# Kernel tuning notes

Measured on AMD Instinct MI355X. Metric: run time of the kernel, lower is better.

## Reference

```python
import jax, jax.numpy as jnp
import numpy as np

D_MODEL = 2048
N_HEAD = 16
D_HEAD = D_MODEL // N_HEAD


def setup_inputs() -> dict:
    key = jax.random.key(0)
    k_x, k_qkv, k_proj = jax.random.split(key, 3)
    x = jax.random.normal(k_x, (2, 2048, D_MODEL), dtype=jnp.float32)
    # nn.Linear weights: out = x @ W.T ; store as [out, in] like torch
    scale = 1.0 / np.sqrt(D_MODEL)
    W_qkv = jax.random.uniform(k_qkv, (3 * D_MODEL, D_MODEL), jnp.float32, -scale, scale)
    W_proj = jax.random.uniform(k_proj, (D_MODEL, D_MODEL), jnp.float32, -scale, scale)
    return {"x": x, "W_qkv": W_qkv, "W_proj": W_proj}


def reference(x, W_qkv, W_proj):
    B, T, C = x.shape
    qkv = jnp.einsum('btc,oc->bto', x, W_qkv)  # [B,T,3C]
    q, k, v = jnp.split(qkv, 3, axis=-1)
    def heads(t):
        return t.reshape(B, T, N_HEAD, D_HEAD).transpose(0, 2, 1, 3)  # [B,H,T,Dh]
    q, k, v = heads(q), heads(k), heads(v)
    att = jnp.einsum('bhqd,bhkd->bhqk', q, k) / jnp.sqrt(jnp.float32(D_HEAD))
    causal = jnp.tril(jnp.ones((T, T), dtype=bool))  # True = keep
    att = jnp.where(causal, att, -jnp.inf)
    att = jax.nn.softmax(att, axis=-1)
    y = jnp.einsum('bhqk,bhkd->bhqd', att, v)
    y = y.transpose(0, 2, 1, 3).reshape(B, T, C)
    return jnp.einsum('btc,oc->bto', y, W_proj)
```

## Files before the change

kernel.cpp:

```cpp
#include <hip/hip_runtime.h>
#include <hip/hip_bf16.h>
#include <stdint.h>


typedef __bf16 bf16x8 __attribute__((ext_vector_type(8)));
typedef float f32x4 __attribute__((ext_vector_type(4)));
typedef unsigned short u16x8 __attribute__((ext_vector_type(8)));
typedef unsigned short u16x4 __attribute__((ext_vector_type(4)));

__device__ __forceinline__ unsigned short f2bf(float f) {
  unsigned int u = __builtin_bit_cast(unsigned int, f);
  u += 0x7fff + ((u >> 16) & 1);
  return (unsigned short)(u >> 16);
}
__device__ __forceinline__ float bf2f(unsigned short u) {
  return __builtin_bit_cast(float, (unsigned int)u << 16);
}

__device__ __forceinline__ u16x8 cvt8(const float* p) {
  f32x4 lo = *(const f32x4*)p;
  f32x4 hi = *(const f32x4*)(p + 4);
  u16x8 r;
#pragma unroll
  for (int j = 0; j < 4; j++) { r[j] = f2bf(lo[j]); r[4 + j] = f2bf(hi[j]); }
  return r;
}

__device__ __forceinline__ void gload16(const void* g, void* l) {
  __builtin_amdgcn_global_load_lds(
      (const __attribute__((address_space(1))) void*)g,
      (__attribute__((address_space(3))) void*)l, 16, 0, 0);
}

__global__ __launch_bounds__(256) void f32_to_bf16(
    const float* __restrict__ src, unsigned short* __restrict__ dst, int n8) {
  int i = blockIdx.x * 256 + threadIdx.x;
  const int stride = gridDim.x * 256;
  for (; i < n8; i += stride) {
    u16x8 v = cvt8(src + (size_t)i * 8);
    *(u16x8*)&dst[(size_t)i * 8] = v;
  }
}

template <bool COF32>
__global__ __launch_bounds__(256) void gemm_bf(
    const unsigned short* __restrict__ A, const unsigned short* __restrict__ B,
    void* __restrict__ Cv, int M, int N, int K) {
  __shared__ __align__(16) unsigned short Alds[128 * 32];
  __shared__ __align__(16) unsigned short Blds[128 * 32];

  const int tid  = threadIdx.x;
  const int lane = tid & 63;
  const int w    = tid >> 6;
  const int ln   = lane & 15;
  const int kq   = lane >> 4;
  const int m0 = blockIdx.y * 128;
  const int n0 = blockIdx.x * 128;
  const int m_base = (w >> 1) * 64;
  const int n_base = (w & 1) * 64;

  f32x4 acc[4][4];
#pragma unroll
  for (int i = 0; i < 4; i++)
#pragma unroll
    for (int j = 0; j < 4; j++) acc[i][j] = {0.f, 0.f, 0.f, 0.f};

  const int c0 = tid;
  const int c1 = tid + 256;
  const unsigned short* Ag0 = A + (size_t)(m0 + (c0 >> 2)) * K + (c0 & 3) * 8;
  const unsigned short* Ag1 = A + (size_t)(m0 + (c1 >> 2)) * K + (c1 & 3) * 8;
  const unsigned short* Bg0 = B + (size_t)(n0 + (c0 >> 2)) * K + (c0 & 3) * 8;
  const unsigned short* Bg1 = B + (size_t)(n0 + (c1 >> 2)) * K + (c1 & 3) * 8;
  unsigned short* lA0 = &Alds[(size_t)w * 512];
  unsigned short* lA1 = &Alds[2048 + (size_t)w * 512];
  unsigned short* lB0 = &Blds[(size_t)w * 512];
  unsigned short* lB1 = &Blds[2048 + (size_t)w * 512];

  const int nk = K >> 5;
  for (int kt = 0; kt < nk; kt++) {
    const int ko = kt * 32;
    gload16(Ag0 + ko, lA0);
    gload16(Ag1 + ko, lA1);
    gload16(Bg0 + ko, lB0);
    gload16(Bg1 + ko, lB1);
    __syncthreads();

    bf16x8 af[4], bfr[4];
#pragma unroll
    for (int i = 0; i < 4; i++)
      af[i] = *(const bf16x8*)&Alds[(m_base + i * 16 + ln) * 32 + kq * 8];
#pragma unroll
    for (int j = 0; j < 4; j++)
      bfr[j] = *(const bf16x8*)&Blds[(n_base + j * 16 + ln) * 32 + kq * 8];
#pragma unroll
    for (int i = 0; i < 4; i++)
#pragma unroll
      for (int j = 0; j < 4; j++)
        acc[i][j] = __builtin_amdgcn_mfma_f32_16x16x32_bf16(af[i], bfr[j], acc[i][j], 0, 0, 0);
    __syncthreads();
  }

#pragma unroll
  for (int i = 0; i < 4; i++) {
    const int row_base = m0 + m_base + i * 16 + kq * 4;
#pragma unroll
    for (int j = 0; j < 4; j++) {
      const int col = n0 + n_base + j * 16 + ln;
#pragma unroll
      for (int r = 0; r < 4; r++) {
        const size_t idx = (size_t)(row_base + r) * N + col;
        if (COF32) ((float*)Cv)[idx] = acc[i][j][r];
        else       ((unsigned short*)Cv)[idx] = f2bf(acc[i][j][r]);
      }
    }
  }
}

#define TSEQ 2048
#define CDIM 2048
#define QKVLD 6144
#define DH 128
#define NEG_BIG (-1.0e30f)
#define K_LD 136
#define VT_LD 76
#define P_LD 72

__global__ __launch_bounds__(512, 4) void attn(
    const unsigned short* __restrict__ qkv,
    unsigned short* __restrict__ y) {
  __shared__ __align__(16) unsigned short Klds[64 * K_LD];
  __shared__ __align__(16) unsigned short Vt[DH * VT_LD];
  __shared__ __align__(16) unsigned short Plds[8 * 16 * P_LD];

  const int tid  = threadIdx.x;
  const int lane = tid & 63;
  const int w    = tid >> 6;
  const int ln   = lane & 15;
  const int kq   = lane >> 4;

  const int idx  = blockIdx.x;
  const int half = idx >> 8;
  const int qbi  = idx & 15;
  const int qb   = half ? qbi : 15 - qbi;
  const int h    = (idx >> 4) & 15;
  const int b    = half;
  const int q0   = qb * 128;
  const int qrow = q0 + w * 16 + ln;

  const size_t baseQ = (size_t)b * TSEQ * QKVLD + (size_t)h * DH;
  const size_t baseK = baseQ + CDIM;
  const size_t baseV = baseQ + 2 * CDIM;

  bf16x8 qf[4];
  {
    const float scale = 0.08838834764831845f;
    const unsigned short* qp = qkv + baseQ + (size_t)qrow * QKVLD + kq * 8;
#pragma unroll
    for (int kc = 0; kc < 4; kc++) {
      u16x8 raw = *(const u16x8*)(qp + kc * 32);
      u16x8 t;
#pragma unroll
      for (int j = 0; j < 8; j++) t[j] = f2bf(bf2f(raw[j]) * scale);
      qf[kc] = __builtin_bit_cast(bf16x8, t);
    }
  }

  const int kRow = tid >> 4;
  const int kCol = (tid & 15) * 8;
  const int vK4  = (tid & 15) * 4;
  const int vD0  = (tid >> 4) * 4;
  const unsigned short* Kg = qkv + baseK + (size_t)kRow * QKVLD + kCol;
  const unsigned short* Vg = qkv + baseV + (size_t)vK4 * QKVLD + vD0;

  u16x8 kreg[2];
  u16x4 vreg[4];
#pragma unroll
  for (int it = 0; it < 2; it++)
    kreg[it] = *(const u16x8*)(Kg + (size_t)(it * 32) * QKVLD);
#pragma unroll
  for (int r = 0; r < 4; r++)
    vreg[r] = *(const u16x4*)(Vg + (size_t)r * QKVLD);

  f32x4 o[8];
#pragma unroll
  for (int i = 0; i < 8; i++) o[i] = {0.f, 0.f, 0.f, 0.f};
  float m = NEG_BIG, l = 0.f;
  unsigned short* pw = &Plds[w * 16 * P_LD];

  const int ktEnd   = 2 * qb + 2;
  const int myKtMax = (q0 + w * 16) >> 6;

  for (int kt = 0; kt < ktEnd; kt++) {
    __syncthreads();

#pragma unroll
    for (int it = 0; it < 2; it++)
      *(u16x8*)&Klds[(kRow + it * 32) * K_LD + kCol] = kreg[it];
#pragma unroll
    for (int j = 0; j < 4; j++) {
      u16x4 t = {vreg[0][j], vreg[1][j], vreg[2][j], vreg[3][j]};
      *(u16x4*)&Vt[(vD0 + j) * VT_LD + vK4] = t;
    }
    __syncthreads();

    if (kt + 1 < ktEnd) {
      const size_t off = (size_t)(kt + 1) * 64 * QKVLD;
#pragma unroll
      for (int it = 0; it < 2; it++)
        kreg[it] = *(const u16x8*)(Kg + off + (size_t)(it * 32) * QKVLD);
#pragma unroll
      for (int r = 0; r < 4; r++)
        vreg[r] = *(const u16x4*)(Vg + off + (size_t)r * QKVLD);
    }

    if (kt > myKtMax) continue;

    f32x4 s[4];
#pragma unroll
    for (int nt = 0; nt < 4; nt++) {
      s[nt] = {0.f, 0.f, 0.f, 0.f};
#pragma unroll
      for (int kc = 0; kc < 4; kc++) {
        bf16x8 kb = *(const bf16x8*)&Klds[(nt * 16 + ln) * K_LD + kc * 32 + kq * 8];
        s[nt] = __builtin_amdgcn_mfma_f32_16x16x32_bf16(kb, qf[kc], s[nt], 0, 0, 0);
      }
    }

    if (kt == myKtMax) {
      const int kbase = kt * 64 + kq * 4;
#pragma unroll
      for (int nt = 0; nt < 4; nt++)
#pragma unroll
        for (int r = 0; r < 4; r++)
          if (kbase + nt * 16 + r > qrow) s[nt][r] = NEG_BIG;
    }

    float mt;
    {
      f32x4 t01 = {fmaxf(s[0][0], s[0][1]), fmaxf(s[0][2], s[0][3]),
                   fmaxf(s[1][0], s[1][1]), fmaxf(s[1][2], s[1][3])};
      f32x4 t23 = {fmaxf(s[2][0], s[2][1]), fmaxf(s[2][2], s[2][3]),
                   fmaxf(s[3][0], s[3][1]), fmaxf(s[3][2], s[3][3])};
      f32x4 t = {fmaxf(t01[0], t01[1]), fmaxf(t01[2], t01[3]),
                 fmaxf(t23[0], t23[1]), fmaxf(t23[2], t23[3])};
      mt = fmaxf(fmaxf(t[0], t[1]), fmaxf(t[2], t[3]));
    }
    mt = fmaxf(mt, __shfl_xor(mt, 16, 64));
    mt = fmaxf(mt, __shfl_xor(mt, 32, 64));

    const bool defer = __all(mt - m <= 8.0f);
    const float mn = defer ? m : fmaxf(m, mt);
    const float alpha = defer ? 1.0f : __expf(m - mn);
    m = mn;

    float ps = 0.f;
#pragma unroll
    for (int nt = 0; nt < 4; nt++) {
      u16x4 pbits;
#pragma unroll
      for (int r = 0; r < 4; r++) {
        const float p = __expf(s[nt][r] - mn);
        ps += p;
        pbits[r] = f2bf(p);
      }
      *(u16x4*)&pw[ln * P_LD + nt * 16 + kq * 4] = pbits;
    }
    ps += __shfl_xor(ps, 16, 64);
    ps += __shfl_xor(ps, 32, 64);
    l = l * alpha + ps;

    if (!defer) {
#pragma unroll
      for (int i = 0; i < 8; i++)
#pragma unroll
        for (int r = 0; r < 4; r++) o[i][r] *= alpha;
    }

    bf16x8 pa[2];
#pragma unroll
    for (int kc = 0; kc < 2; kc++)
      pa[kc] = *(const bf16x8*)&pw[ln * P_LD + kc * 32 + kq * 8];
#pragma unroll
    for (int nt = 0; nt < 8; nt++)
#pragma unroll
      for (int kc = 0; kc < 2; kc++) {
        bf16x8 vb = *(const bf16x8*)&Vt[(nt * 16 + ln) * VT_LD + kc * 32 + kq * 8];
        o[nt] = __builtin_amdgcn_mfma_f32_16x16x32_bf16(vb, pa[kc], o[nt], 0, 0, 0);
      }
  }

  const float inv = 1.f / l;
  unsigned short* yp = y + (size_t)(b * TSEQ + qrow) * CDIM + (size_t)h * DH + kq * 4;
#pragma unroll
  for (int nt = 0; nt < 8; nt++) {
    u16x4 ov;
#pragma unroll
    for (int r = 0; r < 4; r++) ov[r] = f2bf(o[nt][r] * inv);
    *(u16x4*)(yp + nt * 16) = ov;
  }
}

extern "C" void kernel_launch(void* const* d_in, const int* in_sizes, int n_in,
                              void* d_out, int out_size, void* d_ws, size_t ws_size,
                              hipStream_t stream) {
  const float* x     = (const float*)d_in[0];
  const float* Wqkv  = (const float*)d_in[1];
  const float* Wproj = (const float*)d_in[2];
  void* out = d_out;

  unsigned short* qkv = (unsigned short*)d_ws;
  unsigned short* y   = qkv + (size_t)4096 * 6144;
  unsigned short* xbf = y;
  unsigned short* wbf = y + (size_t)4096 * 2048;

  f32_to_bf16<<<dim3(2048), 256, 0, stream>>>(x, xbf, (4096 * 2048) / 8);
  f32_to_bf16<<<dim3(2048), 256, 0, stream>>>(Wqkv, wbf, (6144 * 2048) / 8);
  gemm_bf<false><<<dim3(48, 32), 256, 0, stream>>>(xbf, wbf, qkv, 4096, 6144, 2048);
  f32_to_bf16<<<dim3(2048), 256, 0, stream>>>(Wproj, wbf, (2048 * 2048) / 8);
  attn<<<dim3(512), 512, 0, stream>>>(qkv, y);
  gemm_bf<true><<<dim3(16, 32), 256, 0, stream>>>(y, wbf, out, 4096, 2048, 2048);
}
```

Before: 393.4 us.

## Rewrite GEMM as 256x256 tile, 8-wave, double-buffered pipelined kernel

Replaces the 128x128 single-buffered GEMM with a 256x256 tile, 512-thread kernel that uses K=64 steps and double-buffered LDS. Global-to-LDS loads for the next tile are interleaved with MFMA phases, and the kernel adds setprio, fine-grained barriers and an XOR swizzle to avoid LDS bank conflicts. The aim is to hide memory latency and raise data reuse per block in both projection GEMMs. The trade-off is larger LDS use (128KB per block) and fewer blocks, which lowers occupancy and can leave CUs underfilled on the smaller output-projection GEMM, which now launches only 128 blocks.

```diff
diff --git a/kernel.cpp b/kernel.cpp
--- a/kernel.cpp
+++ b/kernel.cpp
@@ -43,74 +43,146 @@
 }
 
 template <bool COF32>
-__global__ __launch_bounds__(256) void gemm_bf(
+__global__ __launch_bounds__(512, 2) void gemm8(
     const unsigned short* __restrict__ A, const unsigned short* __restrict__ B,
     void* __restrict__ Cv, int M, int N, int K) {
-  __shared__ __align__(16) unsigned short Alds[128 * 32];
-  __shared__ __align__(16) unsigned short Blds[128 * 32];
+  __shared__ __align__(1024) unsigned short As[2][16384];
+  __shared__ __align__(1024) unsigned short Bs[2][16384];
 
   const int tid  = threadIdx.x;
   const int lane = tid & 63;
   const int w    = tid >> 6;
   const int ln   = lane & 15;
   const int kq   = lane >> 4;
-  const int m0 = blockIdx.y * 128;
-  const int n0 = blockIdx.x * 128;
-  const int m_base = (w >> 1) * 64;
-  const int n_base = (w & 1) * 64;
-
-  f32x4 acc[4][4];
-#pragma unroll
-  for (int i = 0; i < 4; i++)
+  const int wm   = w >> 2;
+  const int wn   = w & 3;
+  const int m0 = blockIdx.y * 256;
+  const int n0 = blockIdx.x * 256;
+
+  const int kswz = (kq * 8) ^ ((ln & 4) << 2);
+
+  const int lx = lane ^ (((lane >> 5) & 1) << 1);
+  const int sr = w * 16 + (lx >> 3);
+  const int sk = (lx & 7) * 8;
+  const unsigned short* Asrc = A + (size_t)(m0 + sr) * K + sk;
+  const unsigned short* Bsrc = B + (size_t)(n0 + sr) * K + sk;
+
+  f32x4 acc[8][4];
+#pragma unroll
+  for (int i = 0; i < 8; i++)
 #pragma unroll
     for (int j = 0; j < 4; j++) acc[i][j] = {0.f, 0.f, 0.f, 0.f};
 
-  const int c0 = tid;
-  const int c1 = tid + 256;
-  const unsigned short* Ag0 = A + (size_t)(m0 + (c0 >> 2)) * K + (c0 & 3) * 8;
-  const unsigned short* Ag1 = A + (size_t)(m0 + (c1 >> 2)) * K + (c1 & 3) * 8;
-  const unsigned short* Bg0 = B + (size_t)(n0 + (c0 >> 2)) * K + (c0 & 3) * 8;
-  const unsigned short* Bg1 = B + (size_t)(n0 + (c1 >> 2)) * K + (c1 & 3) * 8;
-  unsigned short* lA0 = &Alds[(size_t)w * 512];
-  unsigned short* lA1 = &Alds[2048 + (size_t)w * 512];
-  unsigned short* lB0 = &Blds[(size_t)w * 512];
-  unsigned short* lB1 = &Blds[2048 + (size_t)w * 512];
-
-  const int nk = K >> 5;
-  for (int kt = 0; kt < nk; kt++) {
-    const int ko = kt * 32;
-    gload16(Ag0 + ko, lA0);
-    gload16(Ag1 + ko, lA1);
-    gload16(Bg0 + ko, lB0);
-    gload16(Bg1 + ko, lB1);
-    __syncthreads();
-
-    bf16x8 af[4], bfr[4];
+  auto stgA = [&](int buf, int t, int h) {
+    const size_t tc = (size_t)t * 64;
+    gload16(Asrc + (size_t)(h * 128) * K + tc,     &As[buf][h * 8192 + (w * 2 + 0) * 512]);
+    gload16(Asrc + (size_t)(h * 128 + 8) * K + tc, &As[buf][h * 8192 + (w * 2 + 1) * 512]);
+  };
+  auto stgB = [&](int buf, int t, int h) {
+    const size_t tc = (size_t)t * 64;
+    gload16(Bsrc + (size_t)(h * 128) * K + tc,     &Bs[buf][h * 8192 + (w * 2 + 0) * 512]);
+    gload16(Bsrc + (size_t)(h * 128 + 8) * K + tc, &Bs[buf][h * 8192 + (w * 2 + 1) * 512]);
+  };
+  auto rdA = [&](int buf, int mi, int ks) -> bf16x8 {
+    return *(const bf16x8*)&As[buf][(wm * 128 + mi * 16 + ln) * 64 + ks * 32 + kswz];
+  };
+  auto rdB = [&](int buf, int nj, int ks) -> bf16x8 {
+    return *(const bf16x8*)&Bs[buf][(wn * 64 + nj * 16 + ln) * 64 + ks * 32 + kswz];
+  };
+
+  const int NT = K >> 6;
+
+  stgA(0, 0, 0); stgA(0, 0, 1); stgB(0, 0, 0); stgB(0, 0, 1);
+  stgA(1, 1, 0); stgA(1, 1, 1);
+  asm volatile("s_waitcnt vmcnt(4)" ::: "memory");
+  __builtin_amdgcn_s_barrier();
+
+  bf16x8 a0[4][2], a1[4][2], b01[2][2], b23[2][2];
+
+#pragma unroll 2
+  for (int t = 0; t < NT; t++) {
+    const int cur = t & 1, nxt = cur ^ 1;
+
+#pragma unroll
+    for (int i = 0; i < 4; i++) { a0[i][0] = rdA(cur, i, 0); a0[i][1] = rdA(cur, i, 1); }
+#pragma unroll
+    for (int j = 0; j < 2; j++) { b01[j][0] = rdB(cur, j, 0); b01[j][1] = rdB(cur, j, 1); }
+    if (t + 1 < NT) stgB(nxt, t + 1, 0);
+    __builtin_amdgcn_s_barrier();
+    asm volatile("s_waitcnt lgkmcnt(0)" ::: "memory");
+    __builtin_amdgcn_sched_barrier(0);
+    __builtin_amdgcn_s_setprio(1);
 #pragma unroll
     for (int i = 0; i < 4; i++)
-      af[i] = *(const bf16x8*)&Alds[(m_base + i * 16 + ln) * 32 + kq * 8];
-#pragma unroll
-    for (int j = 0; j < 4; j++)
-      bfr[j] = *(const bf16x8*)&Blds[(n_base + j * 16 + ln) * 32 + kq * 8];
+#pragma unroll
+      for (int j = 0; j < 2; j++) {
+        acc[i][j] = __builtin_amdgcn_mfma_f32_16x16x32_bf16(a0[i][0], b01[j][0], acc[i][j], 0, 0, 0);
+        acc[i][j] = __builtin_amdgcn_mfma_f32_16x16x32_bf16(a0[i][1], b01[j][1], acc[i][j], 0, 0, 0);
+      }
+    __builtin_amdgcn_s_setprio(0);
+    __builtin_amdgcn_s_barrier();
+
+#pragma unroll
+    for (int j = 0; j < 2; j++) { b23[j][0] = rdB(cur, 2 + j, 0); b23[j][1] = rdB(cur, 2 + j, 1); }
+    if (t + 1 < NT) stgB(nxt, t + 1, 1);
+    __builtin_amdgcn_s_barrier();
+    asm volatile("s_waitcnt lgkmcnt(0)" ::: "memory");
+    __builtin_amdgcn_sched_barrier(0);
+    __builtin_amdgcn_s_setprio(1);
 #pragma unroll
     for (int i = 0; i < 4; i++)
 #pragma unroll
-      for (int j = 0; j < 4; j++)
-        acc[i][j] = __builtin_amdgcn_mfma_f32_16x16x32_bf16(af[i], bfr[j], acc[i][j], 0, 0, 0);
-    __syncthreads();
-  }
-
-#pragma unroll
-  for (int i = 0; i < 4; i++) {
-    const int row_base = m0 + m_base + i * 16 + kq * 4;
-#pragma unroll
-    for (int j = 0; j < 4; j++) {
-      const int col = n0 + n_base + j * 16 + ln;
+      for (int j = 0; j < 2; j++) {
+        acc[i][2 + j] = __builtin_amdgcn_mfma_f32_16x16x32_bf16(a0[i][0], b23[j][0], acc[i][2 + j], 0, 0, 0);
+        acc[i][2 + j] = __builtin_amdgcn_mfma_f32_16x16x32_bf16(a0[i][1], b23[j][1], acc[i][2 + j], 0, 0, 0);
+      }
+    __builtin_amdgcn_s_setprio(0);
+    __builtin_amdgcn_s_barrier();
+
+#pragma unroll
+    for (int i = 0; i < 4; i++) { a1[i][0] = rdA(cur, 4 + i, 0); a1[i][1] = rdA(cur, 4 + i, 1); }
+    __builtin_amdgcn_s_barrier();
+    asm volatile("s_waitcnt lgkmcnt(0)" ::: "memory");
+    __builtin_amdgcn_sched_barrier(0);
+    __builtin_amdgcn_s_setprio(1);
+#pragma unroll
+    for (int i = 0; i < 4; i++)
+#pragma unroll
+      for (int j = 0; j < 2; j++) {
+        acc[4 + i][2 + j] = __builtin_amdgcn_mfma_f32_16x16x32_bf16(a1[i][0], b23[j][0], acc[4 + i][2 + j], 0, 0, 0);
+        acc[4 + i][2 + j] = __builtin_amdgcn_mfma_f32_16x16x32_bf16(a1[i][1], b23[j][1], acc[4 + i][2 + j], 0, 0, 0);
+      }
+    __builtin_amdgcn_s_setprio(0);
+    __builtin_amdgcn_s_barrier();
+
+    if (t + 2 < NT) { stgA(cur, t + 2, 0); stgA(cur, t + 2, 1); }
+    __builtin_amdgcn_s_barrier();
+    __builtin_amdgcn_sched_barrier(0);
+    __builtin_amdgcn_s_setprio(1);
+#pragma unroll
+    for (int i = 0; i < 4; i++)
+#pragma unroll
+      for (int j = 0; j < 2; j++) {
+        acc[4 + i][j] = __builtin_amdgcn_mfma_f32_16x16x32_bf16(a1[i][0], b01[j][0], acc[4 + i][j], 0, 0, 0);
+        acc[4 + i][j] = __builtin_amdgcn_mfma_f32_16x16x32_bf16(a1[i][1], b01[j][1], acc[4 + i][j], 0, 0, 0);
+      }
+    __builtin_amdgcn_s_setprio(0);
+    if (t + 2 < NT) asm volatile("s_waitcnt vmcnt(4)" ::: "memory");
+    else            asm volatile("s_waitcnt vmcnt(0)" ::: "memory");
+    __builtin_amdgcn_s_barrier();
+  }
+
+#pragma unroll
+  for (int mi = 0; mi < 8; mi++) {
+    const int row_base = m0 + wm * 128 + mi * 16 + kq * 4;
+#pragma unroll
+    for (int nj = 0; nj < 4; nj++) {
+      const int col = n0 + wn * 64 + nj * 16 + ln;
 #pragma unroll
       for (int r = 0; r < 4; r++) {
         const size_t idx = (size_t)(row_base + r) * N + col;
-        if (COF32) ((float*)Cv)[idx] = acc[i][j][r];
-        else       ((unsigned short*)Cv)[idx] = f2bf(acc[i][j][r]);
+        if (COF32) ((float*)Cv)[idx] = acc[mi][nj][r];
+        else       ((unsigned short*)Cv)[idx] = f2bf(acc[mi][nj][r]);
       }
     }
   }
@@ -315,8 +387,8 @@
 
   f32_to_bf16<<<dim3(2048), 256, 0, stream>>>(x, xbf, (4096 * 2048) / 8);
   f32_to_bf16<<<dim3(2048), 256, 0, stream>>>(Wqkv, wbf, (6144 * 2048) / 8);
-  gemm_bf<false><<<dim3(48, 32), 256, 0, stream>>>(xbf, wbf, qkv, 4096, 6144, 2048);
+  gemm8<false><<<dim3(24, 16), 512, 0, stream>>>(xbf, wbf, qkv, 4096, 6144, 2048);
   f32_to_bf16<<<dim3(2048), 256, 0, stream>>>(Wproj, wbf, (2048 * 2048) / 8);
   attn<<<dim3(512), 512, 0, stream>>>(qkv, y);
-  gemm_bf<true><<<dim3(16, 32), 256, 0, stream>>>(y, wbf, out, 4096, 2048, 2048);
-}
+  gemm8<true><<<dim3(8, 16), 512, 0, stream>>>(y, wbf, out, 4096, 2048, 2048);
+}
```

Measured after the change: 411.5 us. +4.6%, slower.
